# Optimization experiments

Hardware: AMD Instinct MI355X
Metric: run time of the kernel (lower is better)

## Reference

```python
import jax, jax.numpy as jnp
import numpy as np

N, E, D = 50000, 800000, 128  # nodes, edges, in_dim == out_dim


def setup_inputs() -> dict:
    key = jax.random.key(0)
    ks = jax.random.split(key, 10)
    s = 1.0 / np.sqrt(2 * D)
    t = 1.0 / np.sqrt(D)
    return {
        "x": jax.random.normal(ks[0], (N, D), dtype=jnp.float32),
        "edge_index": jax.random.randint(ks[1], (2, E), 0, N, dtype=jnp.int64),
        # message_net: Linear(2D -> D), ReLU, Linear(D -> D)
        "mW1": jax.random.uniform(ks[2], (2 * D, D), jnp.float32, -s, s),
        "mb1": jax.random.uniform(ks[3], (D,), jnp.float32, -s, s),
        "mW2": jax.random.uniform(ks[4], (D, D), jnp.float32, -t, t),
        "mb2": jax.random.uniform(ks[5], (D,), jnp.float32, -t, t),
        # update_net: Linear(D + D -> D), ReLU, Linear(D -> D)
        "uW1": jax.random.uniform(ks[6], (2 * D, D), jnp.float32, -s, s),
        "ub1": jax.random.uniform(ks[7], (D,), jnp.float32, -s, s),
        "uW2": jax.random.uniform(ks[8], (D, D), jnp.float32, -t, t),
        "ub2": jax.random.uniform(ks[9], (D,), jnp.float32, -t, t),
    }


def reference(x, edge_index, mW1, mb1, mW2, mb2, uW1, ub1, uW2, ub2):
    row, col = edge_index[0], edge_index[1]
    # gather endpoints -> [E, 2D]
    msg_in = jnp.concatenate([x[row], x[col]], axis=-1)
    h = jax.nn.relu(msg_in @ mW1 + mb1)
    messages = h @ mW2 + mb2  # [E, D]
    # scatter-add messages to destination nodes (index_add_ on col)
    aggregated = jax.ops.segment_sum(messages, col, num_segments=x.shape[0])
    upd_in = jnp.concatenate([x, aggregated], axis=-1)  # [N, 2D]
    g = jax.nn.relu(upd_in @ uW1 + ub1)
    return jax.nn.relu(g @ uW2 + ub2)
```

## Files before the change

kernel.cpp:

```cpp
#include <hip/hip_runtime.h>
#include <stdint.h>

typedef unsigned short ushort_t;

#define NNODES 50000
#define NEDGES 800000
#define DD 128
#define EB 128

typedef short bf16x8 __attribute__((ext_vector_type(8)));
typedef float f32x16 __attribute__((ext_vector_type(16)));

#define XH_OFF    0u
#define XL_OFF    12800000u
#define W1P_OFF   25600000u
#define W2P_OFF   25731072u
#define WS_MIN    25796608u
#define DEG_OFF   25796608u
#define ELIST_OFF 25996800u
#define CUR_OFF   29196800u
#define WS_CSR    29396992u

#define PQ_OFF2   0u
#define W1P_OFF2  51200000u
#define U2P_OFF2  51331072u
#define WNP_OFF2  51396608u
#define W2U_OFF2  51527680u
#define VV_OFF2   51593216u
#define DEG_OFF2  51593728u
#define CUR_OFF2  51793920u
#define BSUM_OFF2 51994112u
#define EL_OFF2   51994368u
#define WS_NEW    55194368u
#define WS_NEW2   58394368u

#define NB_SCAN 49

__global__ void zero_kernel(float4* __restrict__ p, int n4) {
    int i = blockIdx.x * blockDim.x + threadIdx.x;
    if (i < n4) p[i] = make_float4(0.f, 0.f, 0.f, 0.f);
}
__global__ void zero_i32(int* __restrict__ p, int n) {
    int i = blockIdx.x * blockDim.x + threadIdx.x;
    if (i < n) p[i] = 0;
}

__device__ inline void bf16_split(float f, ushort_t& hi, ushort_t& lo) {
    uint32_t b = __float_as_uint(f);
    uint32_t hb = b & 0xFFFF0000u;
    hi = (ushort_t)(b >> 16);
    float lof = f - __uint_as_float(hb);
    lo = (ushort_t)(__float_as_uint(lof) >> 16);
}

__global__ void pack_x(const float* __restrict__ x,
                       ushort_t* __restrict__ xh, ushort_t* __restrict__ xl) {
    int i = blockIdx.x * blockDim.x + threadIdx.x;
    if (i >= NNODES * DD) return;
    ushort_t h, l;
    bf16_split(x[i], h, l);
    xh[i] = h; xl[i] = l;
}

__global__ void pack_w(const float* __restrict__ W, ushort_t* __restrict__ wp,
                       int K) {
    int i = blockIdx.x * blockDim.x + threadIdx.x;
    if (i >= K * 128) return;
    int k = i >> 7, n = i & 127;
    int base = (k >> 4) * 4096 + ((((k >> 3) & 1) * 128 + n) << 3) + (k & 7);
    ushort_t h, l;
    bf16_split(W[i], h, l);
    wp[base] = h; wp[base + 2048] = l;
}

__global__ void prep0(const float* __restrict__ mW1, const float* __restrict__ uW2,
                      const float* __restrict__ uW1,
                      ushort_t* __restrict__ w1p, ushort_t* __restrict__ u2p,
                      ushort_t* __restrict__ wnp, int* __restrict__ deg) {
    if (blockIdx.x < 256) {
        int i = blockIdx.x * 256 + threadIdx.x;
        const float* W; ushort_t* wp; int li;
        if (i < 32768)      { W = mW1; wp = w1p; li = i; }
        else if (i < 49152) { W = uW2; wp = u2p; li = i - 32768; }
        else                { W = uW1; wp = wnp; li = i - 49152; }
        int k = li >> 7, n = li & 127;
        int base = (k >> 4) * 4096 + ((((k >> 3) & 1) * 128 + n) << 3) + (k & 7);
        ushort_t h, l;
        bf16_split(W[li], h, l);
        wp[base] = h; wp[base + 2048] = l;
    } else {
        int j = (blockIdx.x - 256) * 256 + threadIdx.x;
        if (j < 50048) deg[j] = 0;
    }
}

__global__ void hist_kernel(const int* __restrict__ ei, int* __restrict__ deg) {
    int i = blockIdx.x * blockDim.x + threadIdx.x;
    if (i < NEDGES) atomicAdd(&deg[ei[NEDGES + i]], 1);
}

__global__ __launch_bounds__(1024)
void scan_kernel(const int* __restrict__ deg, int* __restrict__ cursor) {
    __shared__ int part[1024];
    const int t = threadIdx.x;
    const int CH = 49;
    int s = 0;
#pragma unroll 1
    for (int i = 0; i < CH; ++i) {
        int idx = t * CH + i;
        if (idx < NNODES) s += deg[idx];
    }
    part[t] = s;
    __syncthreads();
    for (int d = 1; d < 1024; d <<= 1) {
        int v = (t >= d) ? part[t - d] : 0;
        __syncthreads();
        part[t] += v;
        __syncthreads();
    }
    int run = (t == 0) ? 0 : part[t - 1];
#pragma unroll 1
    for (int i = 0; i < CH; ++i) {
        int idx = t * CH + i;
        if (idx < NNODES) {
            cursor[idx] = run;
            run += deg[idx];
        }
    }
}

__global__ __launch_bounds__(1024)
void scanA(const int* __restrict__ deg, int* __restrict__ cur,
           int* __restrict__ bsum) {
    __shared__ int sm[1024];
    const int t = threadIdx.x;
    const int idx = blockIdx.x * 1024 + t;
    int d = (idx < NNODES) ? deg[idx] : 0;
    sm[t] = d;
    __syncthreads();
    for (int off = 1; off < 1024; off <<= 1) {
        int v = 0;
        if (t >= off) v = sm[t - off];
        __syncthreads();
        sm[t] += v;
        __syncthreads();
    }
    if (idx < NNODES) cur[idx] = sm[t];
    if (t == 1023) bsum[blockIdx.x] = sm[1023];
}
__global__ void scanB(int* __restrict__ bsum, int nb) {
    if (threadIdx.x == 0) {
        int run = 0;
        for (int i = 0; i < nb; ++i) { int v = bsum[i]; bsum[i] = run; run += v; }
    }
}
__global__ __launch_bounds__(1024)
void scanC(const int* __restrict__ deg, int* __restrict__ cur,
           const int* __restrict__ bsum) {
    const int idx = blockIdx.x * 1024 + threadIdx.x;
    if (idx < NNODES) cur[idx] = cur[idx] - deg[idx] + bsum[blockIdx.x];
}
__global__ __launch_bounds__(1024)
void scanC2(const int* __restrict__ deg, int* __restrict__ cur,
            const int* __restrict__ bsum) {
    int pre = 0;
#pragma unroll 1
    for (int j = 0; j < blockIdx.x; ++j) pre += bsum[j];
    const int idx = blockIdx.x * 1024 + threadIdx.x;
    if (idx < NNODES) cur[idx] = cur[idx] - deg[idx] + pre;
}

__global__ void fill_kernel(const int* __restrict__ ei, int* __restrict__ cursor,
                            int* __restrict__ elist) {
    int i = blockIdx.x * blockDim.x + threadIdx.x;
    if (i < NEDGES) {
        int pos = atomicAdd(&cursor[ei[NEDGES + i]], 1);
        elist[pos] = i;
    }
}
__global__ void fill3_kernel(const int* __restrict__ ei, int* __restrict__ cursor,
                             int* __restrict__ srcs) {
    int i = blockIdx.x * blockDim.x + threadIdx.x;
    if (i < NEDGES) {
        int pos = atomicAdd(&cursor[ei[NEDGES + i]], 1);
        srcs[pos] = ei[i];
    }
}

__global__ void w2u_kernel(const float* __restrict__ W2,
                           const float* __restrict__ U1, float* __restrict__ W2U) {
    int id = blockIdx.x * 256 + threadIdx.x;
    if (id >= 128 * 128) return;
    int i = id >> 7, j = id & 127;
    float s = 0.f;
    for (int k = 0; k < 128; ++k) s += W2[i * 128 + k] * U1[(128 + k) * 128 + j];
    W2U[id] = s;
}
__global__ void vvec_kernel(const float* __restrict__ b2,
                            const float* __restrict__ U1, float* __restrict__ vv) {
    int j = threadIdx.x;
    if (j >= 128) return;
    float s = 0.f;
    for (int k = 0; k < 128; ++k) s += b2[k] * U1[(128 + k) * 128 + j];
    vv[j] = s;
}
__global__ void w2u_vv_pack(const float* __restrict__ W2, const float* __restrict__ b2,
                            const float* __restrict__ U1,
                            ushort_t* __restrict__ wnp2, float* __restrict__ vv) {
    if (blockIdx.x < 64) {
        int id = blockIdx.x * 256 + threadIdx.x;
        int i = id >> 7, j = id & 127;
        float s = 0.f;
        for (int k = 0; k < 128; ++k)
            s += W2[i * 128 + k] * U1[(128 + k) * 128 + j];
        int base = (i >> 4) * 4096 + ((((i >> 3) & 1) * 128 + j) << 3) + (i & 7);
        ushort_t h, l;
        bf16_split(s, h, l);
        wnp2[base] = h; wnp2[base + 2048] = l;
    } else if (threadIdx.x < 128) {
        int j = threadIdx.x;
        float s = 0.f;
        for (int k = 0; k < 128; ++k)
            s += b2[k] * U1[(128 + k) * 128 + j];
        vv[j] = s;
    }
}

__global__ __launch_bounds__(256)
void pq_gemm(const float* __restrict__ x, const ushort_t* __restrict__ w1p,
             const float* __restrict__ b1, float* __restrict__ PQ) {
    __shared__ __align__(16) ushort_t Wst[4096];
    const int t = threadIdx.x, w = t >> 6, l = t & 63;
    const int lh = l >> 5, ln = l & 31;
    const int base = blockIdx.x * 128;
    const int c = blockIdx.y;
    const int row = base + w * 32 + ln;
    const float* ax = x + (size_t)min(row, NNODES - 1) * DD;
    const ushort_t* wt = w1p + c * 8 * 4096;

    f32x16 acc[4];
#pragma unroll
    for (int tt = 0; tt < 4; ++tt)
#pragma unroll
        for (int q = 0; q < 16; ++q) acc[tt][q] = 0.f;

    float4 pfh = *(const float4*)(wt + t * 8);
    float4 pfl = *(const float4*)(wt + 2048 + t * 8);
    for (int u = 0; u < 8; ++u) {
        __syncthreads();
        *(float4*)(Wst + t * 8)        = pfh;
        *(float4*)(Wst + 2048 + t * 8) = pfl;
        float4 a0 = *(const float4*)(ax + u * 16 + lh * 8);
        float4 a1 = *(const float4*)(ax + u * 16 + lh * 8 + 4);
        if (u < 7) {
            pfh = *(const float4*)(wt + (u + 1) * 4096 + t * 8);
            pfl = *(const float4*)(wt + (u + 1) * 4096 + 2048 + t * 8);
        }
        float av[8] = {a0.x, a0.y, a0.z, a0.w, a1.x, a1.y, a1.z, a1.w};
        bf16x8 a_hi, a_lo;
#pragma unroll
        for (int q = 0; q < 8; ++q) {
            ushort_t h, lo16;
            bf16_split(av[q], h, lo16);
            a_hi[q] = (short)h; a_lo[q] = (short)lo16;
        }
        __syncthreads();
#pragma unroll
        for (int tt = 0; tt < 4; ++tt) {
            const int boff = (lh * 128 + tt * 32 + ln) * 8;
            bf16x8 bh = *(const bf16x8*)(Wst + boff);
            bf16x8 bl = *(const bf16x8*)(Wst + 2048 + boff);
            acc[tt] = __builtin_amdgcn_mfma_f32_32x32x16_bf16(a_hi, bh, acc[tt], 0, 0, 0);
            acc[tt] = __builtin_amdgcn_mfma_f32_32x32x16_bf16(a_hi, bl, acc[tt], 0, 0, 0);
            acc[tt] = __builtin_amdgcn_mfma_f32_32x32x16_bf16(a_lo, bh, acc[tt], 0, 0, 0);
        }
    }
    float bias[4];
#pragma unroll
    for (int tt = 0; tt < 4; ++tt)
        bias[tt] = (c == 0) ? b1[tt * 32 + ln] : 0.f;
#pragma unroll
    for (int tt = 0; tt < 4; ++tt) {
#pragma unroll
        for (int r = 0; r < 16; ++r) {
            int mrow = w * 32 + (r & 3) + 8 * (r >> 2) + 4 * lh;
            int n = base + mrow;
            if (n < NNODES)
                PQ[(size_t)n * 256 + c * 128 + tt * 32 + ln] = acc[tt][r] + bias[tt];
        }
    }
}

#define EW_C 4
__global__ __launch_bounds__(256)
void edge_ew(const float* __restrict__ PQ, const int* __restrict__ ei,
             const int* __restrict__ elist, float* Hsum) {
    const int t = threadIdx.x, w = t >> 6, l = t & 63;
    const int start = blockIdx.x * 512 + w * 128;
    if (start >= NEDGES) return;
    const int end = min(start + 128, NEDGES);

    float sx = 0.f, sy = 0.f;
    int cur = -1;
    int rv[EW_C] = {0, 0, 0, 0}, cv[EW_C] = {0, 0, 0, 0};
    float px[EW_C] = {0, 0, 0, 0}, py[EW_C] = {0, 0, 0, 0};
    float qx[EW_C] = {0, 0, 0, 0}, qy[EW_C] = {0, 0, 0, 0};

    const int navail = min(EW_C, end - start);
#pragma unroll
    for (int i = 0; i < EW_C; ++i)
        if (i < navail) {
            int e = elist[start + i];
            rv[i] = ei[e]; cv[i] = ei[NEDGES + e];
        }
#pragma unroll
    for (int i = 0; i < EW_C; ++i)
        if (i < navail) {
            float2 p = *(const float2*)(PQ + (size_t)rv[i] * 256 + 2 * l);
            float2 q = *(const float2*)(PQ + (size_t)cv[i] * 256 + 128 + 2 * l);
            px[i] = p.x; py[i] = p.y; qx[i] = q.x; qy[i] = q.y;
        }

    for (int pos = start; pos < end; pos += EW_C) {
        const int cnt = min(EW_C, end - pos);
        int nn = end - (pos + EW_C);
        nn = nn < 0 ? 0 : (nn > EW_C ? EW_C : nn);
        int nrv[EW_C] = {0, 0, 0, 0}, ncv[EW_C] = {0, 0, 0, 0};
        float npx[EW_C] = {0, 0, 0, 0}, npy[EW_C] = {0, 0, 0, 0};
        float nqx[EW_C] = {0, 0, 0, 0}, nqy[EW_C] = {0, 0, 0, 0};
#pragma unroll
        for (int i = 0; i < EW_C; ++i)
            if (i < nn) {
                int e = elist[pos + EW_C + i];
                nrv[i] = ei[e]; ncv[i] = ei[NEDGES + e];
            }
#pragma unroll
        for (int i = 0; i < EW_C; ++i)
            if (i < nn) {
                float2 p = *(const float2*)(PQ + (size_t)nrv[i] * 256 + 2 * l);
                float2 q = *(const float2*)(PQ + (size_t)ncv[i] * 256 + 128 + 2 * l);
                npx[i] = p.x; npy[i] = p.y; nqx[i] = q.x; nqy[i] = q.y;
            }
#pragma unroll
        for (int i = 0; i < EW_C; ++i)
            if (i < cnt) {
                if (cv[i] != cur) {
                    if (cur >= 0) {
                        atomicAdd(Hsum + (size_t)cur * DD + 2 * l,     sx);
                        atomicAdd(Hsum + (size_t)cur * DD + 2 * l + 1, sy);
                    }
                    sx = 0.f; sy = 0.f; cur = cv[i];
                }
                sx += fmaxf(px[i] + qx[i], 0.f);
                sy += fmaxf(py[i] + qy[i], 0.f);
            }
#pragma unroll
        for (int i = 0; i < EW_C; ++i) {
            rv[i] = nrv[i]; cv[i] = ncv[i];
            px[i] = npx[i]; py[i] = npy[i]; qx[i] = nqx[i]; qy[i] = nqy[i];
        }
    }
    if (cur >= 0) {
        atomicAdd(Hsum + (size_t)cur * DD + 2 * l,     sx);
        atomicAdd(Hsum + (size_t)cur * DD + 2 * l + 1, sy);
    }
}

__global__ __launch_bounds__(256)
void edge_pn2(const float* __restrict__ PQ, const int* __restrict__ srcs,
              const int* __restrict__ endp, const int* __restrict__ deg,
              float* __restrict__ Hsum) {
    const int n = blockIdx.x * 4 + (threadIdx.x >> 6);
    if (n >= NNODES) return;
    const int l = threadIdx.x & 63;
    const int end = endp[n];
    const int start = end - deg[n];

    const float2 q = *(const float2*)(PQ + (size_t)n * 256 + 128 + 2 * l);
    float sx = 0.f, sy = 0.f;

    int s0[4];
    float2 p0[4];
    const int c0 = min(4, end - start);
#pragma unroll
    for (int i = 0; i < 4; ++i) s0[i] = (i < c0) ? srcs[start + i] : 0;
#pragma unroll
    for (int i = 0; i < 4; ++i)
        if (i < c0) p0[i] = *(const float2*)(PQ + (size_t)s0[i] * 256 + 2 * l);

    for (int e = start; e < end; e += 4) {
        const int cnt = min(4, end - e);
        int nn = end - (e + 4);
        nn = nn < 0 ? 0 : (nn > 4 ? 4 : nn);
        int s1[4];
        float2 p1[4];
#pragma unroll
        for (int i = 0; i < 4; ++i) s1[i] = (i < nn) ? srcs[e + 4 + i] : 0;
#pragma unroll
        for (int i = 0; i < 4; ++i)
            if (i < nn) p1[i] = *(const float2*)(PQ + (size_t)s1[i] * 256 + 2 * l);
#pragma unroll
        for (int i = 0; i < 4; ++i)
            if (i < cnt) {
                sx += fmaxf(p0[i].x + q.x, 0.f);
                sy += fmaxf(p0[i].y + q.y, 0.f);
            }
#pragma unroll
        for (int i = 0; i < 4; ++i) { s0[i] = s1[i]; p0[i] = p1[i]; }
    }

    Hsum[(size_t)n * DD + 2 * l]     = sx;
    Hsum[(size_t)n * DD + 2 * l + 1] = sy;
}

__device__ inline int hs_idx(int m, int j) {
    return m * 128 + ((((j >> 2) ^ (m & 31)) << 2) | (j & 3));
}

__global__ __launch_bounds__(128)
void node_mfma2(const float* __restrict__ x, float* outHsum,
                const ushort_t* __restrict__ wnp, const ushort_t* __restrict__ u2p,
                const int* __restrict__ deg, const float* __restrict__ vv,
                const float* __restrict__ ub1, const float* __restrict__ ub2) {
    __shared__ __align__(16) float    Hs[64 * 128];
    __shared__ __align__(16) ushort_t Wst[4096];
    const int t = threadIdx.x, w = t >> 6, l = t & 63;
    const int lh = l >> 5, ln = l & 31;
    const int base = blockIdx.x * 64;
    const int row = base + w * 32 + ln;
    const int rowc = min(row, NNODES - 1);
    const float* ax = x + (size_t)rowc * DD;
    const float* ah = outHsum + (size_t)rowc * DD;

    f32x16 acc[4];
#pragma unroll
    for (int tt = 0; tt < 4; ++tt)
#pragma unroll
        for (int q = 0; q < 16; ++q) acc[tt][q] = 0.f;

    float4 pfh0 = *(const float4*)(wnp + t * 8);
    float4 pfh1 = *(const float4*)(wnp + (t + 128) * 8);
    float4 pfl0 = *(const float4*)(wnp + 2048 + t * 8);
    float4 pfl1 = *(const float4*)(wnp + 2048 + (t + 128) * 8);
    for (int u = 0; u < 16; ++u) {
        __syncthreads();
        *(float4*)(Wst + t * 8)                = pfh0;
        *(float4*)(Wst + (t + 128) * 8)        = pfh1;
        *(float4*)(Wst + 2048 + t * 8)         = pfl0;
        *(float4*)(Wst + 2048 + (t + 128) * 8) = pfl1;
        const int k = u * 16 + lh * 8;
        const float* src = (k < 128) ? (ax + k) : (ah + (k - 128));
        float4 a0 = *(const float4*)(src);
        float4 a1 = *(const float4*)(src + 4);
        if (u < 15) {
            const ushort_t* nx = wnp + (u + 1) * 4096;
            pfh0 = *(const float4*)(nx + t * 8);
            pfh1 = *(const float4*)(nx + (t + 128) * 8);
            pfl0 = *(const float4*)(nx + 2048 + t * 8);
            pfl1 = *(const float4*)(nx + 2048 + (t + 128) * 8);
        }
        float av[8] = {a0.x, a0.y, a0.z, a0.w, a1.x, a1.y, a1.z, a1.w};
        bf16x8 a_hi, a_lo;
#pragma unroll
        for (int q = 0; q < 8; ++q) {
            ushort_t h, lo16;
            bf16_split(av[q], h, lo16);
            a_hi[q] = (short)h; a_lo[q] = (short)lo16;
        }
        __syncthreads();
#pragma unroll
        for (int tt = 0; tt < 4; ++tt) {
            const int boff = (lh * 128 + tt * 32 + ln) * 8;
            bf16x8 bh = *(const bf16x8*)(Wst + boff);
            bf16x8 bl = *(const bf16x8*)(Wst + 2048 + boff);
            acc[tt] = __builtin_amdgcn_mfma_f32_32x32x16_bf16(a_hi, bh, acc[tt], 0, 0, 0);
            acc[tt] = __builtin_amdgcn_mfma_f32_32x32x16_bf16(a_hi, bl, acc[tt], 0, 0, 0);
            acc[tt] = __builtin_amdgcn_mfma_f32_32x32x16_bf16(a_lo, bh, acc[tt], 0, 0, 0);
        }
    }

    float4 p2h0 = *(const float4*)(u2p + t * 8);
    float4 p2h1 = *(const float4*)(u2p + (t + 128) * 8);
    float4 p2l0 = *(const float4*)(u2p + 2048 + t * 8);
    float4 p2l1 = *(const float4*)(u2p + 2048 + (t + 128) * 8);

    float b1v[4], vvv[4];
#pragma unroll
    for (int tt = 0; tt < 4; ++tt) {
        b1v[tt] = ub1[tt * 32 + ln];
        vvv[tt] = vv[tt * 32 + ln];
    }
#pragma unroll
    for (int tt = 0; tt < 4; ++tt) {
#pragma unroll
        for (int r = 0; r < 16; ++r) {
            int mrow = w * 32 + (r & 3) + 8 * (r >> 2) + 4 * lh;
            int n = min(base + mrow, NNODES - 1);
            float dg = (float)deg[n];
            float g = acc[tt][r] + b1v[tt] + dg * vvv[tt];
            Hs[hs_idx(mrow, tt * 32 + ln)] = fmaxf(g, 0.f);
            acc[tt][r] = 0.f;
        }
    }

    for (int u = 0; u < 8; ++u) {
        __syncthreads();
        *(float4*)(Wst + t * 8)                = p2h0;
        *(float4*)(Wst + (t + 128) * 8)        = p2h1;
        *(float4*)(Wst + 2048 + t * 8)         = p2l0;
        *(float4*)(Wst + 2048 + (t + 128) * 8) = p2l1;
        if (u < 7) {
            const ushort_t* nx = u2p + (u + 1) * 4096;
            p2h0 = *(const float4*)(nx + t * 8);
            p2h1 = *(const float4*)(nx + (t + 128) * 8);
            p2l0 = *(const float4*)(nx + 2048 + t * 8);
            p2l1 = *(const float4*)(nx + 2048 + (t + 128) * 8);
        }
        __syncthreads();
        const int m  = w * 32 + ln;
        const int s0 = u * 4 + lh * 2;
        float4 f0 = *(const float4*)(Hs + m * 128 + (((s0    ) ^ ln) << 2));
        float4 f1 = *(const float4*)(Hs + m * 128 + (((s0 + 1) ^ ln) << 2));
        float fv[8] = {f0.x, f0.y, f0.z, f0.w, f1.x, f1.y, f1.z, f1.w};
        bf16x8 a_hi, a_lo;
#pragma unroll
        for (int q = 0; q < 8; ++q) {
            ushort_t h, lo16;
            bf16_split(fv[q], h, lo16);
            a_hi[q] = (short)h; a_lo[q] = (short)lo16;
        }
#pragma unroll
        for (int tt = 0; tt < 4; ++tt) {
            const int boff = (lh * 128 + tt * 32 + ln) * 8;
            bf16x8 bh = *(const bf16x8*)(Wst + boff);
            bf16x8 bl = *(const bf16x8*)(Wst + 2048 + boff);
            acc[tt] = __builtin_amdgcn_mfma_f32_32x32x16_bf16(a_hi, bh, acc[tt], 0, 0, 0);
            acc[tt] = __builtin_amdgcn_mfma_f32_32x32x16_bf16(a_hi, bl, acc[tt], 0, 0, 0);
            acc[tt] = __builtin_amdgcn_mfma_f32_32x32x16_bf16(a_lo, bh, acc[tt], 0, 0, 0);
        }
    }

    float b2v[4];
#pragma unroll
    for (int tt = 0; tt < 4; ++tt) b2v[tt] = ub2[tt * 32 + ln];
#pragma unroll
    for (int tt = 0; tt < 4; ++tt) {
#pragma unroll
        for (int r = 0; r < 16; ++r) {
            int mrow = w * 32 + (r & 3) + 8 * (r >> 2) + 4 * lh;
            int n = base + mrow;
            if (n < NNODES)
                outHsum[(size_t)n * DD + tt * 32 + ln] =
                    fmaxf(acc[tt][r] + b2v[tt], 0.f);
        }
    }
}

__global__ __launch_bounds__(256, 2)
void node_mfma(const float* __restrict__ x, float* outHsum,
               const ushort_t* __restrict__ wnp, const ushort_t* __restrict__ u2p,
               const int* __restrict__ deg, const float* __restrict__ vv,
               const float* __restrict__ ub1, const float* __restrict__ ub2) {
    __shared__ __align__(16) float    Hs2[128 * 128];
    __shared__ __align__(16) ushort_t Wst[4096];
    const int t = threadIdx.x, w = t >> 6, l = t & 63;
    const int lh = l >> 5, ln = l & 31;
    const int base = blockIdx.x * 128;
    const int row = base + w * 32 + ln;
    const int rowc = min(row, NNODES - 1);
    const float* ax = x + (size_t)rowc * DD;
    const float* ah = outHsum + (size_t)rowc * DD;

    f32x16 acc[4];
#pragma unroll
    for (int tt = 0; tt < 4; ++tt)
#pragma unroll
        for (int q = 0; q < 16; ++q) acc[tt][q] = 0.f;

    float4 pfh = *(const float4*)(wnp + t * 8);
    float4 pfl = *(const float4*)(wnp + 2048 + t * 8);
    for (int u = 0; u < 16; ++u) {
        __syncthreads();
        *(float4*)(Wst + t * 8)        = pfh;
        *(float4*)(Wst + 2048 + t * 8) = pfl;
        const int k = u * 16 + lh * 8;
        const float* src = (k < 128) ? (ax + k) : (ah + (k - 128));
        float4 a0 = *(const float4*)(src);
        float4 a1 = *(const float4*)(src + 4);
        if (u < 15) {
            pfh = *(const float4*)(wnp + (u + 1) * 4096 + t * 8);
            pfl = *(const float4*)(wnp + (u + 1) * 4096 + 2048 + t * 8);
        }
        float av[8] = {a0.x, a0.y, a0.z, a0.w, a1.x, a1.y, a1.z, a1.w};
        bf16x8 a_hi, a_lo;
#pragma unroll
        for (int q = 0; q < 8; ++q) {
            ushort_t h, lo16;
            bf16_split(av[q], h, lo16);
            a_hi[q] = (short)h; a_lo[q] = (short)lo16;
        }
        __syncthreads();
#pragma unroll
        for (int tt = 0; tt < 4; ++tt) {
            const int boff = (lh * 128 + tt * 32 + ln) * 8;
            bf16x8 bh = *(const bf16x8*)(Wst + boff);
            bf16x8 bl = *(const bf16x8*)(Wst + 2048 + boff);
            acc[tt] = __builtin_amdgcn_mfma_f32_32x32x16_bf16(a_hi, bh, acc[tt], 0, 0, 0);
            acc[tt] = __builtin_amdgcn_mfma_f32_32x32x16_bf16(a_hi, bl, acc[tt], 0, 0, 0);
            acc[tt] = __builtin_amdgcn_mfma_f32_32x32x16_bf16(a_lo, bh, acc[tt], 0, 0, 0);
        }
    }

    float4 pfh2 = *(const float4*)(u2p + t * 8);
    float4 pfl2 = *(const float4*)(u2p + 2048 + t * 8);

    float b1v[4], vvv[4];
#pragma unroll
    for (int tt = 0; tt < 4; ++tt) {
        b1v[tt] = ub1[tt * 32 + ln];
        vvv[tt] = vv[tt * 32 + ln];
    }
#pragma unroll
    for (int tt = 0; tt < 4; ++tt) {
#pragma unroll
        for (int r = 0; r < 16; ++r) {
            int mrow = w * 32 + (r & 3) + 8 * (r >> 2) + 4 * lh;
            int n = min(base + mrow, NNODES - 1);
            float dg = (float)deg[n];
            float g = acc[tt][r] + b1v[tt] + dg * vvv[tt];
            Hs2[hs_idx(mrow, tt * 32 + ln)] = fmaxf(g, 0.f);
            acc[tt][r] = 0.f;
        }
    }

    for (int u = 0; u < 8; ++u) {
        __syncthreads();
        *(float4*)(Wst + t * 8)        = pfh2;
        *(float4*)(Wst + 2048 + t * 8) = pfl2;
        if (u < 7) {
            pfh2 = *(const float4*)(u2p + (u + 1) * 4096 + t * 8);
            pfl2 = *(const float4*)(u2p + (u + 1) * 4096 + 2048 + t * 8);
        }
        __syncthreads();
        const int m  = w * 32 + ln;
        const int s0 = u * 4 + lh * 2;
        float4 f0 = *(const float4*)(Hs2 + m * 128 + (((s0    ) ^ ln) << 2));
        float4 f1 = *(const float4*)(Hs2 + m * 128 + (((s0 + 1) ^ ln) << 2));
        float fv[8] = {f0.x, f0.y, f0.z, f0.w, f1.x, f1.y, f1.z, f1.w};
        bf16x8 a_hi, a_lo;
#pragma unroll
        for (int q = 0; q < 8; ++q) {
            ushort_t h, lo16;
            bf16_split(fv[q], h, lo16);
            a_hi[q] = (short)h; a_lo[q] = (short)lo16;
        }
#pragma unroll
        for (int tt = 0; tt < 4; ++tt) {
            const int boff = (lh * 128 + tt * 32 + ln) * 8;
            bf16x8 bh = *(const bf16x8*)(Wst + boff);
            bf16x8 bl = *(const bf16x8*)(Wst + 2048 + boff);
            acc[tt] = __builtin_amdgcn_mfma_f32_32x32x16_bf16(a_hi, bh, acc[tt], 0, 0, 0);
            acc[tt] = __builtin_amdgcn_mfma_f32_32x32x16_bf16(a_hi, bl, acc[tt], 0, 0, 0);
            acc[tt] = __builtin_amdgcn_mfma_f32_32x32x16_bf16(a_lo, bh, acc[tt], 0, 0, 0);
        }
    }

    float b2v[4];
#pragma unroll
    for (int tt = 0; tt < 4; ++tt) b2v[tt] = ub2[tt * 32 + ln];
#pragma unroll
    for (int tt = 0; tt < 4; ++tt) {
#pragma unroll
        for (int r = 0; r < 16; ++r) {
            int mrow = w * 32 + (r & 3) + 8 * (r >> 2) + 4 * lh;
            int n = base + mrow;
            if (n < NNODES)
                outHsum[(size_t)n * DD + tt * 32 + ln] =
                    fmaxf(acc[tt][r] + b2v[tt], 0.f);
        }
    }
}

template <int MODE>
__global__ __launch_bounds__(256, 2)
void edge_mfma(const ushort_t* __restrict__ xh, const ushort_t* __restrict__ xl,
               const ushort_t* __restrict__ w1p, const ushort_t* __restrict__ w2p,
               const int* __restrict__ ei, const int* __restrict__ elist,
               const float* __restrict__ b1, const float* __restrict__ b2,
               float* agg) {
    __shared__ __align__(16) float    Hsl[128 * 128];
    __shared__ __align__(16) ushort_t Wst[4096];
    const int t  = threadIdx.x;
    const int w  = t >> 6;
    const int l  = t & 63;
    const int lh = l >> 5;
    const int ln = l & 31;
    int eg;
    if (MODE == 1) eg = elist[blockIdx.x * EB + w * 32 + ln];
    else           eg = blockIdx.x * EB + w * 32 + ln;
    const int rv = ei[eg];
    const int cv = ei[NEDGES + eg];
    float bias1[4], bias2[4];
#pragma unroll
    for (int tt = 0; tt < 4; ++tt) {
        bias1[tt] = b1[tt * 32 + ln];
        bias2[tt] = b2[tt * 32 + ln];
    }
// ... 131 lines not shown
#define AX_WORDS (TE * AX_S)
#define WT_WORDS (KT * DD)
#define SMEM_WORDS (AX_WORDS + WT_WORDS + TE)

__global__ __launch_bounds__(256, 2)
void node_kernel(const float* __restrict__ x,
                 float* aggout,
                 const float* __restrict__ U1, const float* __restrict__ c1,
                 const float* __restrict__ U2, const float* __restrict__ c2) {
    __shared__ float smem[SMEM_WORDS];
    float* Ax = smem;
    float* Hss = smem;
    float* Wt = smem + AX_WORDS;
    const int t = threadIdx.x;
    const int base = blockIdx.x * TE;
    {
        const int e = t & 63;
        const int q = t >> 6;
        const int n = base + e;
        const bool valid = n < NNODES;
        const float* s1 = x + (size_t)n * DD;
        const float* s2 = aggout + (size_t)n * DD;
#pragma unroll
        for (int ci = 0; ci < 16; ++ci) {
            const int k4 = ci * 4 + q;
            float4 v = make_float4(0.f, 0.f, 0.f, 0.f);
            if (valid) {
                if (k4 < 32) v = *(const float4*)(s1 + k4 * 4);
                else         v = *(const float4*)(s2 + (k4 - 32) * 4);
            }
            *(float4*)(Ax + e * AX_S + k4 * 4) = v;
        }
    }
    const int jg = t & 31;
    const int eg2 = t >> 5;
    const int j0 = jg * 4;
    const float4 b1v = *(const float4*)(c1 + j0);
    const float4 b2v = *(const float4*)(c2 + j0);
    float acc[8][4];
#pragma unroll
    for (int i = 0; i < 8; ++i)
        acc[i][0] = acc[i][1] = acc[i][2] = acc[i][3] = 0.f;
    for (int kb = 0; kb < 256 / KT; ++kb) {
        __syncthreads();
        {
            const float* src = U1 + kb * KT * DD;
#pragma unroll
            for (int u = 0; u < 2; ++u) {
                const int f4i = u * 256 + t;
                *(float4*)(Wt + f4i * 4) = *(const float4*)(src + f4i * 4);
            }
        }
        __syncthreads();
        float4 Bc[KT];
#pragma unroll
        for (int kk = 0; kk < KT; ++kk)
            Bc[kk] = *(const float4*)(Wt + kk * DD + j0);
#pragma unroll
        for (int i = 0; i < 8; ++i) {
            const float* arow = Ax + (i * 8 + eg2) * AX_S + kb * KT;
            float a[KT];
#pragma unroll
            for (int kc = 0; kc < KT / 4; ++kc) {
                const float4 av = *(const float4*)(arow + kc * 4);
                a[kc * 4 + 0] = av.x; a[kc * 4 + 1] = av.y;
                a[kc * 4 + 2] = av.z; a[kc * 4 + 3] = av.w;
            }
#pragma unroll
            for (int kk = 0; kk < KT; ++kk) {
                acc[i][0] = fmaf(a[kk], Bc[kk].x, acc[i][0]);
                acc[i][1] = fmaf(a[kk], Bc[kk].y, acc[i][1]);
                acc[i][2] = fmaf(a[kk], Bc[kk].z, acc[i][2]);
                acc[i][3] = fmaf(a[kk], Bc[kk].w, acc[i][3]);
            }
        }
    }
    __syncthreads();
#pragma unroll
    for (int i = 0; i < 8; ++i) {
        float4 h;
        h.x = fmaxf(acc[i][0] + b1v.x, 0.f);
        h.y = fmaxf(acc[i][1] + b1v.y, 0.f);
        h.z = fmaxf(acc[i][2] + b1v.z, 0.f);
        h.w = fmaxf(acc[i][3] + b1v.w, 0.f);
        *(float4*)(Hss + (i * 8 + eg2) * HS_S + j0) = h;
        acc[i][0] = acc[i][1] = acc[i][2] = acc[i][3] = 0.f;
    }
    for (int kb = 0; kb < DD / KT; ++kb) {
        __syncthreads();
        {
            const float* src = U2 + kb * KT * DD;
#pragma unroll
            for (int u = 0; u < 2; ++u) {
                const int f4i = u * 256 + t;
                *(float4*)(Wt + f4i * 4) = *(const float4*)(src + f4i * 4);
            }
        }
        __syncthreads();
        float4 Bc[KT];
#pragma unroll
        for (int kk = 0; kk < KT; ++kk)
            Bc[kk] = *(const float4*)(Wt + kk * DD + j0);
#pragma unroll
        for (int i = 0; i < 8; ++i) {
            const float* arow = Hss + (i * 8 + eg2) * HS_S + kb * KT;
            float a[KT];
#pragma unroll
            for (int kc = 0; kc < KT / 4; ++kc) {
                const float4 av = *(const float4*)(arow + kc * 4);
                a[kc * 4 + 0] = av.x; a[kc * 4 + 1] = av.y;
                a[kc * 4 + 2] = av.z; a[kc * 4 + 3] = av.w;
            }
#pragma unroll
            for (int kk = 0; kk < KT; ++kk) {
                acc[i][0] = fmaf(a[kk], Bc[kk].x, acc[i][0]);
                acc[i][1] = fmaf(a[kk], Bc[kk].y, acc[i][1]);
                acc[i][2] = fmaf(a[kk], Bc[kk].z, acc[i][2]);
                acc[i][3] = fmaf(a[kk], Bc[kk].w, acc[i][3]);
            }
        }
    }
#pragma unroll
    for (int i = 0; i < 8; ++i) {
        const int n = base + i * 8 + eg2;
        if (n < NNODES) {
            float4 o;
            o.x = fmaxf(acc[i][0] + b2v.x, 0.f);
            o.y = fmaxf(acc[i][1] + b2v.y, 0.f);
            o.z = fmaxf(acc[i][2] + b2v.z, 0.f);
            o.w = fmaxf(acc[i][3] + b2v.w, 0.f);
            *(float4*)(aggout + (size_t)n * DD + j0) = o;
        }
    }
}

extern "C" void kernel_launch(void* const* d_in, const int* in_sizes, int n_in,
                              void* d_out, int out_size, void* d_ws, size_t ws_size,
                              hipStream_t stream) {
    const float* x   = (const float*)d_in[0];
    const int*   ei  = (const int*)d_in[1];
    const float* mW1 = (const float*)d_in[2];
    const float* mb1 = (const float*)d_in[3];
    const float* mW2 = (const float*)d_in[4];
    const float* mb2 = (const float*)d_in[5];
    const float* uW1 = (const float*)d_in[6];
    const float* ub1 = (const float*)d_in[7];
    const float* uW2 = (const float*)d_in[8];
    const float* ub2 = (const float*)d_in[9];
    float* out = (float*)d_out;

    const int n4 = NNODES * DD / 4;

    if (ws_size >= (size_t)WS_NEW) {
        float*    PQ   = (float*)((char*)d_ws + PQ_OFF2);
        ushort_t* w1p  = (ushort_t*)((char*)d_ws + W1P_OFF2);
        ushort_t* u2p  = (ushort_t*)((char*)d_ws + U2P_OFF2);
        ushort_t* wnp  = (ushort_t*)((char*)d_ws + WNP_OFF2);
        float*    W2U  = (float*)((char*)d_ws + W2U_OFF2);
        float*    vv   = (float*)((char*)d_ws + VV_OFF2);
        int*      deg  = (int*)((char*)d_ws + DEG_OFF2);
        int*      curb = (int*)((char*)d_ws + CUR_OFF2);
        int*      bsum = (int*)((char*)d_ws + BSUM_OFF2);

        if (ws_size >= (size_t)WS_NEW2) {
            int* srcs = (int*)((char*)d_ws + EL_OFF2);
            prep0<<<452, 256, 0, stream>>>(mW1, uW2, uW1, w1p, u2p, wnp, deg);
            hist_kernel<<<(NEDGES + 255) / 256, 256, 0, stream>>>(ei, deg);
            scanA<<<NB_SCAN, 1024, 0, stream>>>(deg, curb, bsum);
            scanC2<<<NB_SCAN, 1024, 0, stream>>>(deg, curb, bsum);
            fill3_kernel<<<(NEDGES + 255) / 256, 256, 0, stream>>>(ei, curb, srcs);
            w2u_vv_pack<<<65, 256, 0, stream>>>(mW2, mb2, uW1, wnp + 32768, vv);
            pq_gemm<<<dim3(391, 2), 256, 0, stream>>>(x, w1p, mb1, PQ);
            edge_pn2<<<(NNODES + 3) / 4, 256, 0, stream>>>(PQ, srcs, curb, deg, out);
            node_mfma2<<<(NNODES + 63) / 64, 128, 0, stream>>>(
                x, out, wnp, u2p, deg, vv, ub1, ub2);
        } else {
            int* elst = (int*)((char*)d_ws + EL_OFF2);
            zero_kernel<<<(n4 + 255) / 256, 256, 0, stream>>>((float4*)out, n4);
            zero_i32<<<(50048 + 255) / 256, 256, 0, stream>>>(deg, 50048);
            hist_kernel<<<(NEDGES + 255) / 256, 256, 0, stream>>>(ei, deg);
            scanA<<<NB_SCAN, 1024, 0, stream>>>(deg, curb, bsum);
            scanB<<<1, 64, 0, stream>>>(bsum, NB_SCAN);
            scanC<<<NB_SCAN, 1024, 0, stream>>>(deg, curb, bsum);
            fill_kernel<<<(NEDGES + 255) / 256, 256, 0, stream>>>(ei, curb, elst);
            pack_w<<<(256 * 128 + 255) / 256, 256, 0, stream>>>(mW1, w1p, 256);
            pack_w<<<(128 * 128 + 255) / 256, 256, 0, stream>>>(uW2, u2p, 128);
            w2u_kernel<<<64, 256, 0, stream>>>(mW2, uW1, W2U);
            vvec_kernel<<<1, 128, 0, stream>>>(mb2, uW1, vv);
            pack_w<<<(128 * 128 + 255) / 256, 256, 0, stream>>>(uW1, wnp, 128);
            pack_w<<<(128 * 128 + 255) / 256, 256, 0, stream>>>(W2U, wnp + 32768, 128);
            pq_gemm<<<dim3(391, 2), 256, 0, stream>>>(x, w1p, mb1, PQ);
            edge_ew<<<(NEDGES + 511) / 512, 256, 0, stream>>>(PQ, ei, elst, out);
            node_mfma<<<391, 256, 0, stream>>>(x, out, wnp, u2p, deg, vv, ub1, ub2);
        }
        return;
    }

    zero_kernel<<<(n4 + 255) / 256, 256, 0, stream>>>((float4*)out, n4);
    if (ws_size >= (size_t)WS_MIN) {
        ushort_t* xh  = (ushort_t*)((char*)d_ws + XH_OFF);
        ushort_t* xl  = (ushort_t*)((char*)d_ws + XL_OFF);
        ushort_t* w1p = (ushort_t*)((char*)d_ws + W1P_OFF);
        ushort_t* w2p = (ushort_t*)((char*)d_ws + W2P_OFF);
        pack_x<<<(NNODES * DD + 255) / 256, 256, 0, stream>>>(x, xh, xl);
        pack_w<<<(256 * 128 + 255) / 256, 256, 0, stream>>>(mW1, w1p, 256);
        pack_w<<<(128 * 128 + 255) / 256, 256, 0, stream>>>(mW2, w2p, 128);
        if (ws_size >= (size_t)WS_CSR) {
            int* deg    = (int*)((char*)d_ws + DEG_OFF);
            int* elist  = (int*)((char*)d_ws + ELIST_OFF);
            int* cursor = (int*)((char*)d_ws + CUR_OFF);
            zero_i32<<<(50048 + 255) / 256, 256, 0, stream>>>(deg, 50048);
            hist_kernel<<<(NEDGES + 255) / 256, 256, 0, stream>>>(ei, deg);
            scan_kernel<<<1, 1024, 0, stream>>>(deg, cursor);
            fill_kernel<<<(NEDGES + 255) / 256, 256, 0, stream>>>(ei, cursor, elist);
            edge_mfma<1><<<NEDGES / EB, 256, 0, stream>>>(
                xh, xl, w1p, w2p, ei, elist, mb1, mb2, out);
        } else {
            edge_mfma<0><<<NEDGES / EB, 256, 0, stream>>>(
                xh, xl, w1p, w2p, ei, (const int*)nullptr, mb1, mb2, out);
        }
    }
    node_kernel<<<(NNODES + TE - 1) / TE, 256, 0, stream>>>(x, out, uW1, ub1,
                                                            uW2, ub2);
}
```

Before: 315.0 us.

## Store PQ in bf16 and merge fill/hist with GEMM and weight-prep kernels

Stores the node-wise PQ projections as round-to-nearest bf16 instead of fp32, halving the bytes gathered per edge in the CSR edge aggregation kernel. The histogram is merged with the W2·U1 weight-folding kernel, and the CSR fill is merged with the PQ GEMM into single launches, so independent work shares one grid and two launches go away. The cost is reduced precision in the per-edge message inputs (bf16 rounding of P and Q before the ReLU sum), which could affect accuracy tolerance.

```diff
diff --git a/kernel.cpp b/kernel.cpp
--- a/kernel.cpp
+++ b/kernel.cpp
@@ -35,6 +35,7 @@
 #define WS_NEW2   58394368u
 
 #define NB_SCAN 49
+#define FILLB   3125
 
 __global__ void zero_kernel(float4* __restrict__ p, int n4) {
     int i = blockIdx.x * blockDim.x + threadIdx.x;
@@ -51,6 +52,11 @@
     hi = (ushort_t)(b >> 16);
     float lof = f - __uint_as_float(hb);
     lo = (ushort_t)(__float_as_uint(lof) >> 16);
+}
+__device__ inline ushort_t f32_bf16_rn(float f) {
+    uint32_t b = __float_as_uint(f);
+    uint32_t r = b + 0x7FFFu + ((b >> 16) & 1u);
+    return (ushort_t)(r >> 16);
 }
 
 __global__ void pack_x(const float* __restrict__ x,
@@ -99,6 +105,35 @@
     if (i < NEDGES) atomicAdd(&deg[ei[NEDGES + i]], 1);
 }
 
+__global__ void hist_w2u(const int* __restrict__ ei, int* __restrict__ deg,
+                         const float* __restrict__ W2, const float* __restrict__ b2,
+                         const float* __restrict__ U1,
+                         ushort_t* __restrict__ wnp2, float* __restrict__ vv) {
+    if (blockIdx.x < FILLB) {
+        int i = blockIdx.x * 256 + threadIdx.x;
+        if (i < NEDGES) atomicAdd(&deg[ei[NEDGES + i]], 1);
+    } else {
+        int bw = blockIdx.x - FILLB;
+        if (bw < 64) {
+            int id = bw * 256 + threadIdx.x;
+            int i = id >> 7, j = id & 127;
+            float s = 0.f;
+            for (int k = 0; k < 128; ++k)
+                s += W2[i * 128 + k] * U1[(128 + k) * 128 + j];
+            int base = (i >> 4) * 4096 + ((((i >> 3) & 1) * 128 + j) << 3) + (i & 7);
+            ushort_t h, l;
+            bf16_split(s, h, l);
+            wnp2[base] = h; wnp2[base + 2048] = l;
+        } else if (threadIdx.x < 128) {
+            int j = threadIdx.x;
+            float s = 0.f;
+            for (int k = 0; k < 128; ++k)
+                s += b2[k] * U1[(128 + k) * 128 + j];
+            vv[j] = s;
+        }
+    }
+}
+
 __global__ __launch_bounds__(1024)
 void scan_kernel(const int* __restrict__ deg, int* __restrict__ cursor) {
     __shared__ int part[1024];
@@ -178,14 +213,6 @@
         elist[pos] = i;
     }
 }
-__global__ void fill3_kernel(const int* __restrict__ ei, int* __restrict__ cursor,
-                             int* __restrict__ srcs) {
-    int i = blockIdx.x * blockDim.x + threadIdx.x;
-    if (i < NEDGES) {
-        int pos = atomicAdd(&cursor[ei[NEDGES + i]], 1);
-        srcs[pos] = ei[i];
-    }
-}
 
 __global__ void w2u_kernel(const float* __restrict__ W2,
                            const float* __restrict__ U1, float* __restrict__ W2U) {
@@ -204,36 +231,26 @@
     for (int k = 0; k < 128; ++k) s += b2[k] * U1[(128 + k) * 128 + j];
     vv[j] = s;
 }
-__global__ void w2u_vv_pack(const float* __restrict__ W2, const float* __restrict__ b2,
-                            const float* __restrict__ U1,
-                            ushort_t* __restrict__ wnp2, float* __restrict__ vv) {
-    if (blockIdx.x < 64) {
-        int id = blockIdx.x * 256 + threadIdx.x;
-        int i = id >> 7, j = id & 127;
-        float s = 0.f;
-        for (int k = 0; k < 128; ++k)
-            s += W2[i * 128 + k] * U1[(128 + k) * 128 + j];
-        int base = (i >> 4) * 4096 + ((((i >> 3) & 1) * 128 + j) << 3) + (i & 7);
-        ushort_t h, l;
-        bf16_split(s, h, l);
-        wnp2[base] = h; wnp2[base + 2048] = l;
-    } else if (threadIdx.x < 128) {
-        int j = threadIdx.x;
-        float s = 0.f;
-        for (int k = 0; k < 128; ++k)
-            s += b2[k] * U1[(128 + k) * 128 + j];
-        vv[j] = s;
-    }
-}
 
 __global__ __launch_bounds__(256)
-void pq_gemm(const float* __restrict__ x, const ushort_t* __restrict__ w1p,
-             const float* __restrict__ b1, float* __restrict__ PQ) {
+void fill_pq(const int* __restrict__ ei, int* __restrict__ cursor,
+             int* __restrict__ srcs,
+             const float* __restrict__ x, const ushort_t* __restrict__ w1p,
+             const float* __restrict__ b1, ushort_t* __restrict__ PQb) {
     __shared__ __align__(16) ushort_t Wst[4096];
+    if (blockIdx.x < FILLB) {
+        int i = blockIdx.x * 256 + threadIdx.x;
+        if (i < NEDGES) {
+            int pos = atomicAdd(&cursor[ei[NEDGES + i]], 1);
+            srcs[pos] = ei[i];
+        }
+        return;
+    }
+    const int bx2 = blockIdx.x - FILLB;
+    const int c = (bx2 >= 391) ? 1 : 0;
+    const int base = (bx2 - c * 391) * 128;
     const int t = threadIdx.x, w = t >> 6, l = t & 63;
     const int lh = l >> 5, ln = l & 31;
-    const int base = blockIdx.x * 128;
-    const int c = blockIdx.y;
     const int row = base + w * 32 + ln;
     const float* ax = x + (size_t)min(row, NNODES - 1) * DD;
     const ushort_t* wt = w1p + c * 8 * 4096;
@@ -286,88 +303,14 @@
             int mrow = w * 32 + (r & 3) + 8 * (r >> 2) + 4 * lh;
             int n = base + mrow;
             if (n < NNODES)
-                PQ[(size_t)n * 256 + c * 128 + tt * 32 + ln] = acc[tt][r] + bias[tt];
-        }
-    }
-}
-
-#define EW_C 4
+                PQb[(size_t)n * 256 + c * 128 + tt * 32 + ln] =
+                    f32_bf16_rn(acc[tt][r] + bias[tt]);
+        }
+    }
+}
+
 __global__ __launch_bounds__(256)
-void edge_ew(const float* __restrict__ PQ, const int* __restrict__ ei,
-             const int* __restrict__ elist, float* Hsum) {
-    const int t = threadIdx.x, w = t >> 6, l = t & 63;
-    const int start = blockIdx.x * 512 + w * 128;
-    if (start >= NEDGES) return;
-    const int end = min(start + 128, NEDGES);
-
-    float sx = 0.f, sy = 0.f;
-    int cur = -1;
-    int rv[EW_C] = {0, 0, 0, 0}, cv[EW_C] = {0, 0, 0, 0};
-    float px[EW_C] = {0, 0, 0, 0}, py[EW_C] = {0, 0, 0, 0};
-    float qx[EW_C] = {0, 0, 0, 0}, qy[EW_C] = {0, 0, 0, 0};
-
-    const int navail = min(EW_C, end - start);
-#pragma unroll
-    for (int i = 0; i < EW_C; ++i)
-        if (i < navail) {
-            int e = elist[start + i];
-            rv[i] = ei[e]; cv[i] = ei[NEDGES + e];
-        }
-#pragma unroll
-    for (int i = 0; i < EW_C; ++i)
-        if (i < navail) {
-            float2 p = *(const float2*)(PQ + (size_t)rv[i] * 256 + 2 * l);
-            float2 q = *(const float2*)(PQ + (size_t)cv[i] * 256 + 128 + 2 * l);
-            px[i] = p.x; py[i] = p.y; qx[i] = q.x; qy[i] = q.y;
-        }
-
-    for (int pos = start; pos < end; pos += EW_C) {
-        const int cnt = min(EW_C, end - pos);
-        int nn = end - (pos + EW_C);
-        nn = nn < 0 ? 0 : (nn > EW_C ? EW_C : nn);
-        int nrv[EW_C] = {0, 0, 0, 0}, ncv[EW_C] = {0, 0, 0, 0};
-        float npx[EW_C] = {0, 0, 0, 0}, npy[EW_C] = {0, 0, 0, 0};
-        float nqx[EW_C] = {0, 0, 0, 0}, nqy[EW_C] = {0, 0, 0, 0};
-#pragma unroll
-        for (int i = 0; i < EW_C; ++i)
-            if (i < nn) {
-                int e = elist[pos + EW_C + i];
-                nrv[i] = ei[e]; ncv[i] = ei[NEDGES + e];
-            }
-#pragma unroll
-        for (int i = 0; i < EW_C; ++i)
-            if (i < nn) {
-                float2 p = *(const float2*)(PQ + (size_t)nrv[i] * 256 + 2 * l);
-                float2 q = *(const float2*)(PQ + (size_t)ncv[i] * 256 + 128 + 2 * l);
-                npx[i] = p.x; npy[i] = p.y; nqx[i] = q.x; nqy[i] = q.y;
-            }
-#pragma unroll
-        for (int i = 0; i < EW_C; ++i)
-            if (i < cnt) {
-                if (cv[i] != cur) {
-                    if (cur >= 0) {
-                        atomicAdd(Hsum + (size_t)cur * DD + 2 * l,     sx);
-                        atomicAdd(Hsum + (size_t)cur * DD + 2 * l + 1, sy);
-                    }
-                    sx = 0.f; sy = 0.f; cur = cv[i];
-                }
-                sx += fmaxf(px[i] + qx[i], 0.f);
-                sy += fmaxf(py[i] + qy[i], 0.f);
-            }
-#pragma unroll
-        for (int i = 0; i < EW_C; ++i) {
-            rv[i] = nrv[i]; cv[i] = ncv[i];
-            px[i] = npx[i]; py[i] = npy[i]; qx[i] = nqx[i]; qy[i] = nqy[i];
-        }
-    }
-    if (cur >= 0) {
-        atomicAdd(Hsum + (size_t)cur * DD + 2 * l,     sx);
-        atomicAdd(Hsum + (size_t)cur * DD + 2 * l + 1, sy);
-    }
-}
-
-__global__ __launch_bounds__(256)
-void edge_pn2(const float* __restrict__ PQ, const int* __restrict__ srcs,
+void edge_pnb(const ushort_t* __restrict__ PQb, const int* __restrict__ srcs,
               const int* __restrict__ endp, const int* __restrict__ deg,
               float* __restrict__ Hsum) {
     const int n = blockIdx.x * 4 + (threadIdx.x >> 6);
@@ -376,34 +319,40 @@
     const int end = endp[n];
     const int start = end - deg[n];
 
-    const float2 q = *(const float2*)(PQ + (size_t)n * 256 + 128 + 2 * l);
+    const uint32_t qp = *(const uint32_t*)(PQb + (size_t)n * 256 + 128 + 2 * l);
+    const float qx = __uint_as_float(qp << 16);
+    const float qy = __uint_as_float(qp & 0xFFFF0000u);
     float sx = 0.f, sy = 0.f;
 
     int s0[4];
-    float2 p0[4];
+    uint32_t p0[4];
     const int c0 = min(4, end - start);
 #pragma unroll
     for (int i = 0; i < 4; ++i) s0[i] = (i < c0) ? srcs[start + i] : 0;
 #pragma unroll
     for (int i = 0; i < 4; ++i)
-        if (i < c0) p0[i] = *(const float2*)(PQ + (size_t)s0[i] * 256 + 2 * l);
+        if (i < c0) p0[i] = *(const uint32_t*)(PQb + (size_t)s0[i] * 256 + 2 * l);
 
     for (int e = start; e < end; e += 4) {
         const int cnt = min(4, end - e);
         int nn = end - (e + 4);
         nn = nn < 0 ? 0 : (nn > 4 ? 4 : nn);
         int s1[4];
-        float2 p1[4];
+        uint32_t p1[4];
 #pragma unroll
         for (int i = 0; i < 4; ++i) s1[i] = (i < nn) ? srcs[e + 4 + i] : 0;
 #pragma unroll
-        for (int i = 0; i < 4; ++i)
-            if (i < nn) p1[i] = *(const float2*)(PQ + (size_t)s1[i] * 256 + 2 * l);
+        for (int i = 0; i < 4; ++i) {
+            p1[i] = 0;
+            if (i < nn) p1[i] = *(const uint32_t*)(PQb + (size_t)s1[i] * 256 + 2 * l);
+        }
 #pragma unroll
         for (int i = 0; i < 4; ++i)
             if (i < cnt) {
-                sx += fmaxf(p0[i].x + q.x, 0.f);
-                sy += fmaxf(p0[i].y + q.y, 0.f);
+                float px = __uint_as_float(p0[i] << 16);
+                float py = __uint_as_float(p0[i] & 0xFFFF0000u);
+                sx += fmaxf(px + qx, 0.f);
+                sy += fmaxf(py + qy, 0.f);
             }
 #pragma unroll
         for (int i = 0; i < 4; ++i) { s0[i] = s1[i]; p0[i] = p1[i]; }
@@ -553,6 +502,146 @@
                 outHsum[(size_t)n * DD + tt * 32 + ln] =
                     fmaxf(acc[tt][r] + b2v[tt], 0.f);
         }
+    }
+}
+
+__global__ __launch_bounds__(256)
+void pq_gemm(const float* __restrict__ x, const ushort_t* __restrict__ w1p,
+             const float* __restrict__ b1, float* __restrict__ PQ) {
+    __shared__ __align__(16) ushort_t Wst[4096];
+    const int t = threadIdx.x, w = t >> 6, l = t & 63;
+    const int lh = l >> 5, ln = l & 31;
+    const int base = blockIdx.x * 128;
+    const int c = blockIdx.y;
+    const int row = base + w * 32 + ln;
+    const float* ax = x + (size_t)min(row, NNODES - 1) * DD;
+    const ushort_t* wt = w1p + c * 8 * 4096;
+
+    f32x16 acc[4];
+#pragma unroll
+    for (int tt = 0; tt < 4; ++tt)
+#pragma unroll
+        for (int q = 0; q < 16; ++q) acc[tt][q] = 0.f;
+
+    float4 pfh = *(const float4*)(wt + t * 8);
+    float4 pfl = *(const float4*)(wt + 2048 + t * 8);
+    for (int u = 0; u < 8; ++u) {
+        __syncthreads();
+        *(float4*)(Wst + t * 8)        = pfh;
+        *(float4*)(Wst + 2048 + t * 8) = pfl;
+        float4 a0 = *(const float4*)(ax + u * 16 + lh * 8);
+        float4 a1 = *(const float4*)(ax + u * 16 + lh * 8 + 4);
+        if (u < 7) {
+            pfh = *(const float4*)(wt + (u + 1) * 4096 + t * 8);
+            pfl = *(const float4*)(wt + (u + 1) * 4096 + 2048 + t * 8);
+        }
+        float av[8] = {a0.x, a0.y, a0.z, a0.w, a1.x, a1.y, a1.z, a1.w};
+        bf16x8 a_hi, a_lo;
+#pragma unroll
+        for (int q = 0; q < 8; ++q) {
+            ushort_t h, lo16;
+            bf16_split(av[q], h, lo16);
+            a_hi[q] = (short)h; a_lo[q] = (short)lo16;
+        }
+        __syncthreads();
+#pragma unroll
+        for (int tt = 0; tt < 4; ++tt) {
+            const int boff = (lh * 128 + tt * 32 + ln) * 8;
+            bf16x8 bh = *(const bf16x8*)(Wst + boff);
+            bf16x8 bl = *(const bf16x8*)(Wst + 2048 + boff);
+            acc[tt] = __builtin_amdgcn_mfma_f32_32x32x16_bf16(a_hi, bh, acc[tt], 0, 0, 0);
+            acc[tt] = __builtin_amdgcn_mfma_f32_32x32x16_bf16(a_hi, bl, acc[tt], 0, 0, 0);
+            acc[tt] = __builtin_amdgcn_mfma_f32_32x32x16_bf16(a_lo, bh, acc[tt], 0, 0, 0);
+        }
+    }
+    float bias[4];
+#pragma unroll
+    for (int tt = 0; tt < 4; ++tt)
+        bias[tt] = (c == 0) ? b1[tt * 32 + ln] : 0.f;
+#pragma unroll
+    for (int tt = 0; tt < 4; ++tt) {
+#pragma unroll
+        for (int r = 0; r < 16; ++r) {
+            int mrow = w * 32 + (r & 3) + 8 * (r >> 2) + 4 * lh;
+            int n = base + mrow;
+            if (n < NNODES)
+                PQ[(size_t)n * 256 + c * 128 + tt * 32 + ln] = acc[tt][r] + bias[tt];
+        }
+    }
+}
+
+#define EW_C 4
+__global__ __launch_bounds__(256)
+void edge_ew(const float* __restrict__ PQ, const int* __restrict__ ei,
+             const int* __restrict__ elist, float* Hsum) {
+    const int t = threadIdx.x, w = t >> 6, l = t & 63;
+    const int start = blockIdx.x * 512 + w * 128;
+    if (start >= NEDGES) return;
+    const int end = min(start + 128, NEDGES);
+
+    float sx = 0.f, sy = 0.f;
+    int cur = -1;
+    int rv[EW_C] = {0, 0, 0, 0}, cv[EW_C] = {0, 0, 0, 0};
+    float px[EW_C] = {0, 0, 0, 0}, py[EW_C] = {0, 0, 0, 0};
+    float qx[EW_C] = {0, 0, 0, 0}, qy[EW_C] = {0, 0, 0, 0};
+
+    const int navail = min(EW_C, end - start);
+#pragma unroll
+    for (int i = 0; i < EW_C; ++i)
+        if (i < navail) {
+            int e = elist[start + i];
+            rv[i] = ei[e]; cv[i] = ei[NEDGES + e];
+        }
+#pragma unroll
+    for (int i = 0; i < EW_C; ++i)
+        if (i < navail) {
+            float2 p = *(const float2*)(PQ + (size_t)rv[i] * 256 + 2 * l);
+            float2 q = *(const float2*)(PQ + (size_t)cv[i] * 256 + 128 + 2 * l);
+            px[i] = p.x; py[i] = p.y; qx[i] = q.x; qy[i] = q.y;
+        }
+
+    for (int pos = start; pos < end; pos += EW_C) {
+        const int cnt = min(EW_C, end - pos);
+        int nn = end - (pos + EW_C);
+        nn = nn < 0 ? 0 : (nn > EW_C ? EW_C : nn);
+        int nrv[EW_C] = {0, 0, 0, 0}, ncv[EW_C] = {0, 0, 0, 0};
+        float npx[EW_C] = {0, 0, 0, 0}, npy[EW_C] = {0, 0, 0, 0};
+        float nqx[EW_C] = {0, 0, 0, 0}, nqy[EW_C] = {0, 0, 0, 0};
+#pragma unroll
+        for (int i = 0; i < EW_C; ++i)
+            if (i < nn) {
+                int e = elist[pos + EW_C + i];
+                nrv[i] = ei[e]; ncv[i] = ei[NEDGES + e];
+            }
+#pragma unroll
+        for (int i = 0; i < EW_C; ++i)
+            if (i < nn) {
+                float2 p = *(const float2*)(PQ + (size_t)nrv[i] * 256 + 2 * l);
+                float2 q = *(const float2*)(PQ + (size_t)ncv[i] * 256 + 128 + 2 * l);
+                npx[i] = p.x; npy[i] = p.y; nqx[i] = q.x; nqy[i] = q.y;
+            }
+#pragma unroll
+        for (int i = 0; i < EW_C; ++i)
+            if (i < cnt) {
+                if (cv[i] != cur) {
+                    if (cur >= 0) {
+                        atomicAdd(Hsum + (size_t)cur * DD + 2 * l,     sx);
+                        atomicAdd(Hsum + (size_t)cur * DD + 2 * l + 1, sy);
+                    }
+                    sx = 0.f; sy = 0.f; cur = cv[i];
+                }
+                sx += fmaxf(px[i] + qx[i], 0.f);
+                sy += fmaxf(py[i] + qy[i], 0.f);
+            }
+#pragma unroll
+        for (int i = 0; i < EW_C; ++i) {
+            rv[i] = nrv[i]; cv[i] = ncv[i];
+            px[i] = npx[i]; py[i] = npy[i]; qx[i] = nqx[i]; qy[i] = nqy[i];
+        }
+    }
+    if (cur >= 0) {
+        atomicAdd(Hsum + (size_t)cur * DD + 2 * l,     sx);
+        atomicAdd(Hsum + (size_t)cur * DD + 2 * l + 1, sy);
     }
 }
 
@@ -990,7 +1079,6 @@
     const int n4 = NNODES * DD / 4;
 
     if (ws_size >= (size_t)WS_NEW) {
-        float*    PQ   = (float*)((char*)d_ws + PQ_OFF2);
         ushort_t* w1p  = (ushort_t*)((char*)d_ws + W1P_OFF2);
         ushort_t* u2p  = (ushort_t*)((char*)d_ws + U2P_OFF2);
         ushort_t* wnp  = (ushort_t*)((char*)d_ws + WNP_OFF2);
@@ -1001,19 +1089,21 @@
         int*      bsum = (int*)((char*)d_ws + BSUM_OFF2);
 
         if (ws_size >= (size_t)WS_NEW2) {
-            int* srcs = (int*)((char*)d_ws + EL_OFF2);
+            ushort_t* PQb  = (ushort_t*)((char*)d_ws + PQ_OFF2);
+            int*      srcs = (int*)((char*)d_ws + EL_OFF2);
             prep0<<<452, 256, 0, stream>>>(mW1, uW2, uW1, w1p, u2p, wnp, deg);
-            hist_kernel<<<(NEDGES + 255) / 256, 256, 0, stream>>>(ei, deg);
+            hist_w2u<<<FILLB + 65, 256, 0, stream>>>(ei, deg, mW2, mb2, uW1,
+                                                     wnp + 32768, vv);
             scanA<<<NB_SCAN, 1024, 0, stream>>>(deg, curb, bsum);
             scanC2<<<NB_SCAN, 1024, 0, stream>>>(deg, curb, bsum);
-            fill3_kernel<<<(NEDGES + 255) / 256, 256, 0, stream>>>(ei, curb, srcs);
-            w2u_vv_pack<<<65, 256, 0, stream>>>(mW2, mb2, uW1, wnp + 32768, vv);
-            pq_gemm<<<dim3(391, 2), 256, 0, stream>>>(x, w1p, mb1, PQ);
-            edge_pn2<<<(NNODES + 3) / 4, 256, 0, stream>>>(PQ, srcs, curb, deg, out);
+            fill_pq<<<FILLB + 782, 256, 0, stream>>>(ei, curb, srcs, x, w1p,
+                                                     mb1, PQb);
+            edge_pnb<<<(NNODES + 3) / 4, 256, 0, stream>>>(PQb, srcs, curb, deg, out);
             node_mfma2<<<(NNODES + 63) / 64, 128, 0, stream>>>(
                 x, out, wnp, u2p, deg, vv, ub1, ub2);
         } else {
-            int* elst = (int*)((char*)d_ws + EL_OFF2);
+            float* PQ   = (float*)((char*)d_ws + PQ_OFF2);
+            int*   elst = (int*)((char*)d_ws + EL_OFF2);
             zero_kernel<<<(n4 + 255) / 256, 256, 0, stream>>>((float4*)out, n4);
             zero_i32<<<(50048 + 255) / 256, 256, 0, stream>>>(deg, 50048);
             hist_kernel<<<(NEDGES + 255) / 256, 256, 0, stream>>>(ei, deg);
```

Measured after the change: 325.6 us. +3.4%, slower.
